# Optimization experiments

Hardware: AMD Instinct MI355X
Metric: run time of the kernel (lower is better)

## Reference

```python
import jax, jax.numpy as jnp
import numpy as np


def setup_inputs() -> dict:
    key = jax.random.key(0)
    ks = jax.random.split(key, 8)
    B, C, H, W = 4, 256, 64, 64
    C8 = C // 8
    s = 0.05
    return {
        "x": jax.random.normal(ks[0], (B, C, H, W), jnp.float32),
        "wq": jax.random.normal(ks[1], (C8, C), jnp.float32) * s,
        "bq": jax.random.normal(ks[2], (C8,), jnp.float32) * s,
        "wk": jax.random.normal(ks[3], (C8, C), jnp.float32) * s,
        "bk": jax.random.normal(ks[4], (C8,), jnp.float32) * s,
        "wv": jax.random.normal(ks[5], (C, C), jnp.float32) * s,
        "bv": jax.random.normal(ks[6], (C,), jnp.float32) * s,
        "gamma": jax.random.uniform(ks[7], (1,), jnp.float32),
    }


def reference(x, wq, bq, wk, bk, wv, bv, gamma):
    B, C, H, W = x.shape
    N = H * W
    xf = x.reshape(B, C, N)  # flatten spatial: [B, C, N]
    # 1x1 convs are channel-wise matmuls
    q = jnp.einsum("dc,bcn->bnd", wq, xf) + bq[None, None, :]  # [B, N, C/8]
    k = jnp.einsum("dc,bcn->bdn", wk, xf) + bk[None, :, None]  # [B, C/8, N]
    v = jnp.einsum("dc,bcn->bdn", wv, xf) + bv[None, :, None]  # [B, C, N]
    energy = jnp.einsum("bnd,bdm->bnm", q, k)  # [B, N, N]
    attention = jax.nn.softmax(energy, axis=-1)
    # out = value @ attention^T  -> [B, C, N]
    out = jnp.einsum("bcm,bnm->bcn", v, attention)
    out = out.reshape(B, C, H, W)
    return gamma[0] * out + x
```

## Files before the change

kernel.cpp:

```cpp
#include <hip/hip_runtime.h>
#include <hip/hip_bf16.h>
#include <stdint.h>

#define B_ 4
#define C_ 256
#define N_ 4096
#define D_ 32
#define KT 512

typedef __bf16 bf16_t;
typedef __bf16 bf16x4_t __attribute__((ext_vector_type(4)));
typedef __bf16 bf16x8_t __attribute__((ext_vector_type(8)));
typedef float  f32x4    __attribute__((ext_vector_type(4)));

__global__ __launch_bounds__(256) void cast_w_kernel(
    const float* __restrict__ wq, const float* __restrict__ wk,
    const float* __restrict__ wv, bf16_t* __restrict__ Wb)
{
  const int gr = blockIdx.x;
  const int t  = threadIdx.x;
  float v;
  if (gr < 32)      v = wq[gr * C_ + t];
  else if (gr < 64) v = wk[(gr - 32) * C_ + t];
  else              v = wv[(gr - 64) * C_ + t];
  Wb[gr * C_ + t] = (bf16_t)v;
}

__global__ __launch_bounds__(256) void proj_kernel(
    const float* __restrict__ x, const bf16_t* __restrict__ Wb,
    const float* __restrict__ bq, const float* __restrict__ bk,
    const float* __restrict__ bv,
    bf16_t* __restrict__ Qh, bf16_t* __restrict__ Kh, bf16_t* __restrict__ Vh)
{
  __shared__ float xs[64][65];
  const int bi = blockIdx.x;
  const int b  = bi & 3;
  const int n0 = (bi >> 2) * 64;
  const int t = threadIdx.x, w = t >> 6, lane = t & 63;
  const int l4 = lane >> 4, lm = lane & 15;

  const f32x4 z4 = {0.f, 0.f, 0.f, 0.f};
  f32x4 acc[5][4];
#pragma unroll
  for (int rt = 0; rt < 5; ++rt)
#pragma unroll
    for (int ct = 0; ct < 4; ++ct) acc[rt][ct] = z4;

  const int lr = t >> 2;
  const int lc = (t & 3) * 16;

#pragma unroll 1
  for (int k0 = 0; k0 < C_; k0 += 64) {
    __syncthreads();
#pragma unroll
    for (int i = 0; i < 4; ++i) {
      const f32x4 v = *(const f32x4*)(x + ((size_t)(b * C_ + k0 + lr)) * N_ + n0 + lc + i * 4);
      xs[lr][lc + i * 4 + 0] = v[0];
      xs[lr][lc + i * 4 + 1] = v[1];
      xs[lr][lc + i * 4 + 2] = v[2];
      xs[lr][lc + i * 4 + 3] = v[3];
    }
    __syncthreads();

    bf16x8_t af[5][2], bfr[4][2];
#pragma unroll
    for (int rt = 0; rt < 5; ++rt)
#pragma unroll
      for (int kc = 0; kc < 2; ++kc)
        af[rt][kc] = *(const bf16x8_t*)(Wb + (size_t)(w * 80 + rt * 16 + lm) * C_ + k0 + kc * 32 + l4 * 8);
#pragma unroll
    for (int ct = 0; ct < 4; ++ct)
#pragma unroll
      for (int kc = 0; kc < 2; ++kc) {
        bf16_t tmp[8];
#pragma unroll
        for (int j = 0; j < 8; ++j)
          tmp[j] = (bf16_t)xs[kc * 32 + l4 * 8 + j][ct * 16 + lm];
        bfr[ct][kc] = *(bf16x8_t*)tmp;
      }
#pragma unroll
    for (int rt = 0; rt < 5; ++rt)
#pragma unroll
      for (int ct = 0; ct < 4; ++ct)
#pragma unroll
        for (int kc = 0; kc < 2; ++kc)
          acc[rt][ct] = __builtin_amdgcn_mfma_f32_16x16x32_bf16(af[rt][kc], bfr[ct][kc], acc[rt][ct], 0, 0, 0);
  }

#pragma unroll
  for (int rt = 0; rt < 5; ++rt)
#pragma unroll
    for (int r = 0; r < 4; ++r) {
      const int gr = w * 80 + rt * 16 + 4 * l4 + r;
      const float bias = (gr < 32) ? bq[gr] : (gr < 64) ? bk[gr - 32] : bv[gr - 64];
#pragma unroll
      for (int ct = 0; ct < 4; ++ct) {
        const int n = n0 + ct * 16 + lm;
        float v = acc[rt][ct][r] + bias;
        if (gr < 32) {
          v *= 1.44269504088896f;
          Qh[((size_t)(b * N_ + n)) * D_ + gr] = (bf16_t)v;
        } else if (gr < 64) {
          Kh[((size_t)(b * N_ + n)) * D_ + (gr - 32)] = (bf16_t)v;
        } else {
          Vh[((size_t)(b * C_ + (gr - 64))) * N_ + n] = (bf16_t)v;
        }
      }
    }
}

__global__ __launch_bounds__(512, 2) void attn_kernel(
    const bf16_t* __restrict__ Qh, const bf16_t* __restrict__ Kh,
    const bf16_t* __restrict__ Vh, const float* __restrict__ x,
    const float* __restrict__ gamma, float* __restrict__ out)
{
  __shared__ __align__(16) bf16_t Pl[2][64][KT];
  __shared__ __align__(16) float  Lx[64][12];

  const int bi = blockIdx.x;
  const int xcd = bi & 7, slot = bi >> 3;
  const int b  = xcd >> 1;
  const int q0 = ((xcd & 1) * 32 + slot) * 64;

  const int t = threadIdx.x, w = t >> 6, lane = t & 63;
  const int l4 = lane >> 4, lm = lane & 15;
  const int swz = (lm & 7) << 3;

  const f32x4 z4 = {0.f, 0.f, 0.f, 0.f};

  bf16x8_t qf[4];
#pragma unroll
  for (int rt = 0; rt < 4; ++rt)
    qf[rt] = *(const bf16x8_t*)(Qh + ((size_t)(b * N_ + q0 + rt * 16 + lm)) * D_ + l4 * 8);

  const bf16_t* kbase = Kh + ((size_t)(b * N_ + w * 64 + lm)) * D_ + l4 * 8;
  const bf16_t* vbase = Vh + ((size_t)(b * C_ + w * 32 + lm)) * N_ + l4 * 8;

  f32x4 acc[2][4];
#pragma unroll
  for (int ct = 0; ct < 2; ++ct)
#pragma unroll
    for (int rt = 0; rt < 4; ++rt) acc[ct][rt] = z4;
  float l_run[4] = {0.f, 0.f, 0.f, 0.f};

  bf16x8_t kf[4], kn[4];
#pragma unroll
  for (int mt = 0; mt < 4; ++mt)
    kf[mt] = *(const bf16x8_t*)(kbase + (size_t)(mt * 16) * D_);
  bf16x8_t vf0[2][2], vf1[2][2];
#pragma unroll
  for (int ct = 0; ct < 2; ++ct)
#pragma unroll
    for (int kc = 0; kc < 2; ++kc) {
      vf0[ct][kc] = *(const bf16x8_t*)(vbase + (size_t)(ct * 16) * N_ + kc * 32);
      vf1[ct][kc] = *(const bf16x8_t*)(vbase + (size_t)(ct * 16) * N_ + 64 + kc * 32);
    }

#pragma unroll 1
  for (int it = 0; it < N_ / KT; ++it) {
    const int buf = it & 1;

    f32x4 S[4][4];
#pragma unroll
    for (int rt = 0; rt < 4; ++rt)
#pragma unroll
      for (int mt = 0; mt < 4; ++mt)
        S[rt][mt] = __builtin_amdgcn_mfma_f32_16x16x32_bf16(kf[mt], qf[rt], z4, 0, 0, 0);

    const int k0n = ((it + 1) * KT) & (N_ - 1);
#pragma unroll
    for (int mt = 0; mt < 4; ++mt)
      kn[mt] = *(const bf16x8_t*)(kbase + (size_t)(k0n + mt * 16) * D_);

#pragma unroll
    for (int rt = 0; rt < 4; ++rt) {
      const int prow = rt * 16 + lm;
#pragma unroll
      for (int mt = 0; mt < 4; ++mt) {
        const float p0 = __builtin_amdgcn_exp2f(S[rt][mt][0]);
        const float p1 = __builtin_amdgcn_exp2f(S[rt][mt][1]);
        const float p2 = __builtin_amdgcn_exp2f(S[rt][mt][2]);
        const float p3 = __builtin_amdgcn_exp2f(S[rt][mt][3]);
        l_run[rt] += (p0 + p1) + (p2 + p3);
        bf16x4_t w4 = {(bf16_t)p0, (bf16_t)p1, (bf16_t)p2, (bf16_t)p3};
        *(bf16x4_t*)&Pl[buf][prow][(w * 64 + mt * 16 + 4 * l4) ^ swz] = w4;
      }
    }

    asm volatile("s_waitcnt lgkmcnt(0)" ::: "memory");
    __builtin_amdgcn_s_barrier();

#pragma unroll
    for (int s4 = 0; s4 < 8; ++s4) {
      bf16x8_t pa[4][2];
#pragma unroll
      for (int rt = 0; rt < 4; ++rt)
#pragma unroll
        for (int kc = 0; kc < 2; ++kc)
          pa[rt][kc] = *(const bf16x8_t*)&Pl[buf][rt * 16 + lm][(s4 * 64 + kc * 32 + l4 * 8) ^ swz];
      const int knx = (it * KT + (s4 + 2) * 64) & (N_ - 1);
      if ((s4 & 1) == 0) {
#pragma unroll
        for (int ct = 0; ct < 2; ++ct)
#pragma unroll
          for (int kc = 0; kc < 2; ++kc)
#pragma unroll
            for (int rt = 0; rt < 4; ++rt)
              acc[ct][rt] = __builtin_amdgcn_mfma_f32_16x16x32_bf16(vf0[ct][kc], pa[rt][kc], acc[ct][rt], 0, 0, 0);
#pragma unroll
        for (int ct = 0; ct < 2; ++ct)
#pragma unroll
          for (int kc = 0; kc < 2; ++kc)
            vf0[ct][kc] = *(const bf16x8_t*)(vbase + (size_t)(ct * 16) * N_ + knx + kc * 32);
      } else {
#pragma unroll
        for (int ct = 0; ct < 2; ++ct)
#pragma unroll
          for (int kc = 0; kc < 2; ++kc)
#pragma unroll
            for (int rt = 0; rt < 4; ++rt)
              acc[ct][rt] = __builtin_amdgcn_mfma_f32_16x16x32_bf16(vf1[ct][kc], pa[rt][kc], acc[ct][rt], 0, 0, 0);
#pragma unroll
        for (int ct = 0; ct < 2; ++ct)
#pragma unroll
          for (int kc = 0; kc < 2; ++kc)
            vf1[ct][kc] = *(const bf16x8_t*)(vbase + (size_t)(ct * 16) * N_ + knx + kc * 32);
      }
    }

#pragma unroll
    for (int mt = 0; mt < 4; ++mt) kf[mt] = kn[mt];
  }

#pragma unroll
  for (int rt = 0; rt < 4; ++rt) {
    l_run[rt] += __shfl_xor(l_run[rt], 16);
    l_run[rt] += __shfl_xor(l_run[rt], 32);
  }
  if (l4 == 0) {
#pragma unroll
    for (int rt = 0; rt < 4; ++rt) Lx[rt * 16 + lm][w] = l_run[rt];
  }
  asm volatile("s_waitcnt lgkmcnt(0)" ::: "memory");
  __builtin_amdgcn_s_barrier();

  const float g = gamma[0];
#pragma unroll
  for (int rt = 0; rt < 4; ++rt) {
    const f32x4 s0 = *(const f32x4*)&Lx[rt * 16 + lm][0];
    const f32x4 s1 = *(const f32x4*)&Lx[rt * 16 + lm][4];
    const float lt = ((s0[0] + s0[1]) + (s0[2] + s0[3])) + ((s1[0] + s1[1]) + (s1[2] + s1[3]));
    const float inv = 1.f / lt;
    const int n = q0 + rt * 16 + lm;
#pragma unroll
    for (int ct = 0; ct < 2; ++ct) {
#pragma unroll
      for (int r = 0; r < 4; ++r) {
        const int c = w * 32 + ct * 16 + 4 * l4 + r;
        const size_t idx = ((size_t)(b * C_ + c)) * N_ + n;
        out[idx] = g * (acc[ct][rt][r] * inv) + x[idx];
      }
    }
  }
}

extern "C" void kernel_launch(void* const* d_in, const int* in_sizes, int n_in,
                              void* d_out, int out_size, void* d_ws, size_t ws_size,
                              hipStream_t stream) {
  const float* x     = (const float*)d_in[0];
  const float* wq    = (const float*)d_in[1];
  const float* bq    = (const float*)d_in[2];
  const float* wk    = (const float*)d_in[3];
  const float* bk    = (const float*)d_in[4];
  const float* wv    = (const float*)d_in[5];
  const float* bv    = (const float*)d_in[6];
  const float* gamma = (const float*)d_in[7];
  float* out = (float*)d_out;

  bf16_t* Qh = (bf16_t*)d_ws;
  bf16_t* Kh = Qh + (size_t)B_ * N_ * D_;
  bf16_t* Vh = Kh + (size_t)B_ * N_ * D_;
  bf16_t* Wb = Vh + (size_t)B_ * C_ * N_;

  cast_w_kernel<<<320, 256, 0, stream>>>(wq, wk, wv, Wb);
  proj_kernel<<<256, 256, 0, stream>>>(x, Wb, bq, bk, bv, Qh, Kh, Vh);
  attn_kernel<<<256, 512, 0, stream>>>(Qh, Kh, Vh, x, gamma, out);
}
```

Baseline: 93.12 us.

## Split attention work across 16 waves with key-split PV and LDS reduction

Doubles the attention block to 1024 threads and halves the key tile to 256. Each wave now computes one 16-key slice of the score tile instead of 64 keys. In the PV stage, wave pairs split the key dimension, and their partial accumulators are reduced through LDS before the epilogue. The aim is more waves in flight per CU to hide latency, at the cost of twice as many barriers per key, fewer MFMAs between barriers, an extra reduction pass, and the loss of the 2-blocks-per-CU occupancy hint.

```diff
diff --git a/kernel.cpp b/kernel.cpp
--- a/kernel.cpp
+++ b/kernel.cpp
@@ -6,7 +6,7 @@
 #define C_ 256
 #define N_ 4096
 #define D_ 32
-#define KT 512
+#define KT 256
 
 typedef __bf16 bf16_t;
 typedef __bf16 bf16x4_t __attribute__((ext_vector_type(4)));
@@ -109,13 +109,13 @@
     }
 }
 
-__global__ __launch_bounds__(512, 2) void attn_kernel(
+__global__ __launch_bounds__(1024) void attn_kernel(
     const bf16_t* __restrict__ Qh, const bf16_t* __restrict__ Kh,
     const bf16_t* __restrict__ Vh, const float* __restrict__ x,
     const float* __restrict__ gamma, float* __restrict__ out)
 {
   __shared__ __align__(16) bf16_t Pl[2][64][KT];
-  __shared__ __align__(16) float  Lx[64][12];
+  __shared__ __align__(16) float  Lx[64][20];
 
   const int bi = blockIdx.x;
   const int xcd = bi & 7, slot = bi >> 3;
@@ -124,6 +124,7 @@
 
   const int t = threadIdx.x, w = t >> 6, lane = t & 63;
   const int l4 = lane >> 4, lm = lane & 15;
+  const int cg = w >> 1, kh = w & 1;
   const int swz = (lm & 7) << 3;
 
   const f32x4 z4 = {0.f, 0.f, 0.f, 0.f};
@@ -133,8 +134,8 @@
   for (int rt = 0; rt < 4; ++rt)
     qf[rt] = *(const bf16x8_t*)(Qh + ((size_t)(b * N_ + q0 + rt * 16 + lm)) * D_ + l4 * 8);
 
-  const bf16_t* kbase = Kh + ((size_t)(b * N_ + w * 64 + lm)) * D_ + l4 * 8;
-  const bf16_t* vbase = Vh + ((size_t)(b * C_ + w * 32 + lm)) * N_ + l4 * 8;
+  const bf16_t* kbase = Kh + ((size_t)(b * N_ + w * 16 + lm)) * D_ + l4 * 8;
+  const bf16_t* vbase = Vh + ((size_t)(b * C_ + cg * 32 + lm)) * N_ + kh * 128 + l4 * 8;
 
   f32x4 acc[2][4];
 #pragma unroll
@@ -143,93 +144,72 @@
     for (int rt = 0; rt < 4; ++rt) acc[ct][rt] = z4;
   float l_run[4] = {0.f, 0.f, 0.f, 0.f};
 
-  bf16x8_t kf[4], kn[4];
-#pragma unroll
-  for (int mt = 0; mt < 4; ++mt)
-    kf[mt] = *(const bf16x8_t*)(kbase + (size_t)(mt * 16) * D_);
-  bf16x8_t vf0[2][2], vf1[2][2];
-#pragma unroll
-  for (int ct = 0; ct < 2; ++ct)
-#pragma unroll
-    for (int kc = 0; kc < 2; ++kc) {
-      vf0[ct][kc] = *(const bf16x8_t*)(vbase + (size_t)(ct * 16) * N_ + kc * 32);
-      vf1[ct][kc] = *(const bf16x8_t*)(vbase + (size_t)(ct * 16) * N_ + 64 + kc * 32);
-    }
+  bf16x8_t kf;
+  kf = *(const bf16x8_t*)(kbase);
+  bf16x8_t vf0[2], vf1[2];
+#pragma unroll
+  for (int ct = 0; ct < 2; ++ct) {
+    vf0[ct] = *(const bf16x8_t*)(vbase + (size_t)(ct * 16) * N_);
+    vf1[ct] = *(const bf16x8_t*)(vbase + (size_t)(ct * 16) * N_ + 32);
+  }
 
 #pragma unroll 1
   for (int it = 0; it < N_ / KT; ++it) {
     const int buf = it & 1;
 
-    f32x4 S[4][4];
+    f32x4 S[4];
 #pragma unroll
     for (int rt = 0; rt < 4; ++rt)
-#pragma unroll
-      for (int mt = 0; mt < 4; ++mt)
-        S[rt][mt] = __builtin_amdgcn_mfma_f32_16x16x32_bf16(kf[mt], qf[rt], z4, 0, 0, 0);
+      S[rt] = __builtin_amdgcn_mfma_f32_16x16x32_bf16(kf, qf[rt], z4, 0, 0, 0);
 
     const int k0n = ((it + 1) * KT) & (N_ - 1);
-#pragma unroll
-    for (int mt = 0; mt < 4; ++mt)
-      kn[mt] = *(const bf16x8_t*)(kbase + (size_t)(k0n + mt * 16) * D_);
+    bf16x8_t kn = *(const bf16x8_t*)(kbase + (size_t)k0n * D_);
 
 #pragma unroll
     for (int rt = 0; rt < 4; ++rt) {
       const int prow = rt * 16 + lm;
-#pragma unroll
-      for (int mt = 0; mt < 4; ++mt) {
-        const float p0 = __builtin_amdgcn_exp2f(S[rt][mt][0]);
-        const float p1 = __builtin_amdgcn_exp2f(S[rt][mt][1]);
-        const float p2 = __builtin_amdgcn_exp2f(S[rt][mt][2]);
-        const float p3 = __builtin_amdgcn_exp2f(S[rt][mt][3]);
-        l_run[rt] += (p0 + p1) + (p2 + p3);
-        bf16x4_t w4 = {(bf16_t)p0, (bf16_t)p1, (bf16_t)p2, (bf16_t)p3};
-        *(bf16x4_t*)&Pl[buf][prow][(w * 64 + mt * 16 + 4 * l4) ^ swz] = w4;
-      }
+      const float p0 = __builtin_amdgcn_exp2f(S[rt][0]);
+      const float p1 = __builtin_amdgcn_exp2f(S[rt][1]);
+      const float p2 = __builtin_amdgcn_exp2f(S[rt][2]);
+      const float p3 = __builtin_amdgcn_exp2f(S[rt][3]);
+      l_run[rt] += (p0 + p1) + (p2 + p3);
+      bf16x4_t w4 = {(bf16_t)p0, (bf16_t)p1, (bf16_t)p2, (bf16_t)p3};
+      *(bf16x4_t*)&Pl[buf][prow][(w * 16 + 4 * l4) ^ swz] = w4;
     }
 
     asm volatile("s_waitcnt lgkmcnt(0)" ::: "memory");
     __builtin_amdgcn_s_barrier();
 
 #pragma unroll
-    for (int s4 = 0; s4 < 8; ++s4) {
-      bf16x8_t pa[4][2];
+    for (int s4 = 0; s4 < 4; ++s4) {
+      bf16x8_t pa[4];
 #pragma unroll
       for (int rt = 0; rt < 4; ++rt)
-#pragma unroll
-        for (int kc = 0; kc < 2; ++kc)
-          pa[rt][kc] = *(const bf16x8_t*)&Pl[buf][rt * 16 + lm][(s4 * 64 + kc * 32 + l4 * 8) ^ swz];
-      const int knx = (it * KT + (s4 + 2) * 64) & (N_ - 1);
+        pa[rt] = *(const bf16x8_t*)&Pl[buf][rt * 16 + lm][(kh * 128 + s4 * 32 + l4 * 8) ^ swz];
+      const int knx = (it * KT + (s4 + 2) * 32) & 127;
+      const int kbase_nx = ((it + (s4 >= 2)) * KT) & (N_ - 1);
       if ((s4 & 1) == 0) {
 #pragma unroll
         for (int ct = 0; ct < 2; ++ct)
 #pragma unroll
-          for (int kc = 0; kc < 2; ++kc)
-#pragma unroll
-            for (int rt = 0; rt < 4; ++rt)
-              acc[ct][rt] = __builtin_amdgcn_mfma_f32_16x16x32_bf16(vf0[ct][kc], pa[rt][kc], acc[ct][rt], 0, 0, 0);
-#pragma unroll
-        for (int ct = 0; ct < 2; ++ct)
-#pragma unroll
-          for (int kc = 0; kc < 2; ++kc)
-            vf0[ct][kc] = *(const bf16x8_t*)(vbase + (size_t)(ct * 16) * N_ + knx + kc * 32);
+          for (int rt = 0; rt < 4; ++rt)
+            acc[ct][rt] = __builtin_amdgcn_mfma_f32_16x16x32_bf16(vf0[ct], pa[rt], acc[ct][rt], 0, 0, 0);
+#pragma unroll
+        for (int ct = 0; ct < 2; ++ct)
+          vf0[ct] = *(const bf16x8_t*)(vbase + (size_t)(ct * 16) * N_ + kbase_nx + knx);
       } else {
 #pragma unroll
         for (int ct = 0; ct < 2; ++ct)
 #pragma unroll
-          for (int kc = 0; kc < 2; ++kc)
-#pragma unroll
-            for (int rt = 0; rt < 4; ++rt)
-              acc[ct][rt] = __builtin_amdgcn_mfma_f32_16x16x32_bf16(vf1[ct][kc], pa[rt][kc], acc[ct][rt], 0, 0, 0);
-#pragma unroll
-        for (int ct = 0; ct < 2; ++ct)
-#pragma unroll
-          for (int kc = 0; kc < 2; ++kc)
-            vf1[ct][kc] = *(const bf16x8_t*)(vbase + (size_t)(ct * 16) * N_ + knx + kc * 32);
-      }
-    }
-
-#pragma unroll
-    for (int mt = 0; mt < 4; ++mt) kf[mt] = kn[mt];
+          for (int rt = 0; rt < 4; ++rt)
+            acc[ct][rt] = __builtin_amdgcn_mfma_f32_16x16x32_bf16(vf1[ct], pa[rt], acc[ct][rt], 0, 0, 0);
+#pragma unroll
+        for (int ct = 0; ct < 2; ++ct)
+          vf1[ct] = *(const bf16x8_t*)(vbase + (size_t)(ct * 16) * N_ + kbase_nx + knx);
+      }
+    }
+
+    kf = kn;
   }
 
 #pragma unroll
@@ -241,24 +221,42 @@
 #pragma unroll
     for (int rt = 0; rt < 4; ++rt) Lx[rt * 16 + lm][w] = l_run[rt];
   }
+
+  float* Ax = (float*)&Pl[0][0][0];
   asm volatile("s_waitcnt lgkmcnt(0)" ::: "memory");
   __builtin_amdgcn_s_barrier();
 
-  const float g = gamma[0];
-#pragma unroll
-  for (int rt = 0; rt < 4; ++rt) {
-    const f32x4 s0 = *(const f32x4*)&Lx[rt * 16 + lm][0];
-    const f32x4 s1 = *(const f32x4*)&Lx[rt * 16 + lm][4];
-    const float lt = ((s0[0] + s0[1]) + (s0[2] + s0[3])) + ((s1[0] + s1[1]) + (s1[2] + s1[3]));
-    const float inv = 1.f / lt;
-    const int n = q0 + rt * 16 + lm;
-#pragma unroll
-    for (int ct = 0; ct < 2; ++ct) {
-#pragma unroll
-      for (int r = 0; r < 4; ++r) {
-        const int c = w * 32 + ct * 16 + 4 * l4 + r;
-        const size_t idx = ((size_t)(b * C_ + c)) * N_ + n;
-        out[idx] = g * (acc[ct][rt][r] * inv) + x[idx];
+  if (kh == 1) {
+#pragma unroll
+    for (int rt = 0; rt < 4; ++rt)
+#pragma unroll
+      for (int ct = 0; ct < 2; ++ct)
+        *(f32x4*)&Ax[((cg * 64) + rt * 16 + lm) * 32 + ct * 16 + 4 * l4] = acc[ct][rt];
+  }
+  asm volatile("s_waitcnt lgkmcnt(0)" ::: "memory");
+  __builtin_amdgcn_s_barrier();
+
+  if (kh == 0) {
+    const float g = gamma[0];
+#pragma unroll
+    for (int rt = 0; rt < 4; ++rt) {
+      const f32x4 s0 = *(const f32x4*)&Lx[rt * 16 + lm][0];
+      const f32x4 s1 = *(const f32x4*)&Lx[rt * 16 + lm][4];
+      const f32x4 s2 = *(const f32x4*)&Lx[rt * 16 + lm][8];
+      const f32x4 s3 = *(const f32x4*)&Lx[rt * 16 + lm][12];
+      const float lt = (((s0[0] + s0[1]) + (s0[2] + s0[3])) + ((s1[0] + s1[1]) + (s1[2] + s1[3]))) +
+                       (((s2[0] + s2[1]) + (s2[2] + s2[3])) + ((s3[0] + s3[1]) + (s3[2] + s3[3])));
+      const float inv = 1.f / lt;
+      const int n = q0 + rt * 16 + lm;
+#pragma unroll
+      for (int ct = 0; ct < 2; ++ct) {
+        const f32x4 other = *(const f32x4*)&Ax[((cg * 64) + rt * 16 + lm) * 32 + ct * 16 + 4 * l4];
+#pragma unroll
+        for (int r = 0; r < 4; ++r) {
+          const int c = cg * 32 + ct * 16 + 4 * l4 + r;
+          const size_t idx = ((size_t)(b * C_ + c)) * N_ + n;
+          out[idx] = g * ((acc[ct][rt][r] + other[r]) * inv) + x[idx];
+        }
       }
     }
   }
@@ -284,5 +282,5 @@
 
   cast_w_kernel<<<320, 256, 0, stream>>>(wq, wk, wv, Wb);
   proj_kernel<<<256, 256, 0, stream>>>(x, Wb, bq, bk, bv, Qh, Kh, Vh);
-  attn_kernel<<<256, 512, 0, stream>>>(Qh, Kh, Vh, x, gamma, out);
-}
+  attn_kernel<<<256, 1024, 0, stream>>>(Qh, Kh, Vh, x, gamma, out);
+}
```

Result: slower. 96.36 us (+3.5%).

## Software-pipeline QK^T and exp with PV MFMAs using halved key tile

Applied to the files above, without the earlier changes.

Halves the key tile to 256 and restructures the main loop so that the next tile's QK^T MFMAs and exp/P-store run interleaved with the current tile's PV MFMAs. A prologue computes the first P tile and an epilogue drains the last. The intent is to overlap transcendental and LDS-write work with matrix-core work and to need only one barrier per smaller tile. In exchange the loop has more iterations and more barriers overall, and the staged S registers raise register pressure.

```diff
diff --git a/kernel.cpp b/kernel.cpp
--- a/kernel.cpp
+++ b/kernel.cpp
@@ -6,7 +6,7 @@
 #define C_ 256
 #define N_ 4096
 #define D_ 32
-#define KT 512
+#define KT 256
 
 typedef __bf16 bf16_t;
 typedef __bf16 bf16x4_t __attribute__((ext_vector_type(4)));
@@ -133,7 +133,7 @@
   for (int rt = 0; rt < 4; ++rt)
     qf[rt] = *(const bf16x8_t*)(Qh + ((size_t)(b * N_ + q0 + rt * 16 + lm)) * D_ + l4 * 8);
 
-  const bf16_t* kbase = Kh + ((size_t)(b * N_ + w * 64 + lm)) * D_ + l4 * 8;
+  const bf16_t* kbase = Kh + ((size_t)(b * N_ + w * 32 + lm)) * D_ + l4 * 8;
   const bf16_t* vbase = Vh + ((size_t)(b * C_ + w * 32 + lm)) * N_ + l4 * 8;
 
   f32x4 acc[2][4];
@@ -143,10 +143,13 @@
     for (int rt = 0; rt < 4; ++rt) acc[ct][rt] = z4;
   float l_run[4] = {0.f, 0.f, 0.f, 0.f};
 
-  bf16x8_t kf[4], kn[4];
-#pragma unroll
-  for (int mt = 0; mt < 4; ++mt)
+  bf16x8_t kf[2], kn[2];
+#pragma unroll
+  for (int mt = 0; mt < 2; ++mt)
     kf[mt] = *(const bf16x8_t*)(kbase + (size_t)(mt * 16) * D_);
+#pragma unroll
+  for (int mt = 0; mt < 2; ++mt)
+    kn[mt] = *(const bf16x8_t*)(kbase + (size_t)(KT + mt * 16) * D_);
   bf16x8_t vf0[2][2], vf1[2][2];
 #pragma unroll
   for (int ct = 0; ct < 2; ++ct)
@@ -156,49 +159,171 @@
       vf1[ct][kc] = *(const bf16x8_t*)(vbase + (size_t)(ct * 16) * N_ + 64 + kc * 32);
     }
 
+  f32x4 S[4][2];
+#pragma unroll
+  for (int rt = 0; rt < 4; ++rt)
+#pragma unroll
+    for (int mt = 0; mt < 2; ++mt)
+      S[rt][mt] = __builtin_amdgcn_mfma_f32_16x16x32_bf16(kf[mt], qf[rt], z4, 0, 0, 0);
+#pragma unroll
+  for (int rt = 0; rt < 4; ++rt) {
+    const int prow = rt * 16 + lm;
+#pragma unroll
+    for (int mt = 0; mt < 2; ++mt) {
+      const float p0 = __builtin_amdgcn_exp2f(S[rt][mt][0]);
+      const float p1 = __builtin_amdgcn_exp2f(S[rt][mt][1]);
+      const float p2 = __builtin_amdgcn_exp2f(S[rt][mt][2]);
+      const float p3 = __builtin_amdgcn_exp2f(S[rt][mt][3]);
+      l_run[rt] += (p0 + p1) + (p2 + p3);
+      bf16x4_t w4 = {(bf16_t)p0, (bf16_t)p1, (bf16_t)p2, (bf16_t)p3};
+      *(bf16x4_t*)&Pl[0][prow][(w * 32 + mt * 16 + 4 * l4) ^ swz] = w4;
+    }
+  }
+  asm volatile("s_waitcnt lgkmcnt(0)" ::: "memory");
+  __builtin_amdgcn_s_barrier();
+
 #pragma unroll 1
-  for (int it = 0; it < N_ / KT; ++it) {
+  for (int it = 0; it < N_ / KT - 1; ++it) {
     const int buf = it & 1;
-
-    f32x4 S[4][4];
+    bf16x8_t pa[4][2];
+
 #pragma unroll
     for (int rt = 0; rt < 4; ++rt)
 #pragma unroll
-      for (int mt = 0; mt < 4; ++mt)
-        S[rt][mt] = __builtin_amdgcn_mfma_f32_16x16x32_bf16(kf[mt], qf[rt], z4, 0, 0, 0);
-
-    const int k0n = ((it + 1) * KT) & (N_ - 1);
-#pragma unroll
-    for (int mt = 0; mt < 4; ++mt)
-      kn[mt] = *(const bf16x8_t*)(kbase + (size_t)(k0n + mt * 16) * D_);
-
-#pragma unroll
-    for (int rt = 0; rt < 4; ++rt) {
+      for (int kc = 0; kc < 2; ++kc)
+        pa[rt][kc] = *(const bf16x8_t*)&Pl[buf][rt * 16 + lm][(0 * 64 + kc * 32 + l4 * 8) ^ swz];
+#pragma unroll
+    for (int rt = 0; rt < 4; ++rt)
+#pragma unroll
+      for (int mt = 0; mt < 2; ++mt)
+        S[rt][mt] = __builtin_amdgcn_mfma_f32_16x16x32_bf16(kn[mt], qf[rt], z4, 0, 0, 0);
+#pragma unroll
+    for (int ct = 0; ct < 2; ++ct)
+#pragma unroll
+      for (int kc = 0; kc < 2; ++kc)
+#pragma unroll
+        for (int rt = 0; rt < 4; ++rt)
+          acc[ct][rt] = __builtin_amdgcn_mfma_f32_16x16x32_bf16(vf0[ct][kc], pa[rt][kc], acc[ct][rt], 0, 0, 0);
+    {
+      const int knx = (it * KT + 2 * 64) & (N_ - 1);
+#pragma unroll
+      for (int ct = 0; ct < 2; ++ct)
+#pragma unroll
+        for (int kc = 0; kc < 2; ++kc)
+          vf0[ct][kc] = *(const bf16x8_t*)(vbase + (size_t)(ct * 16) * N_ + knx + kc * 32);
+    }
+
+#pragma unroll
+    for (int rt = 0; rt < 4; ++rt)
+#pragma unroll
+      for (int kc = 0; kc < 2; ++kc)
+        pa[rt][kc] = *(const bf16x8_t*)&Pl[buf][rt * 16 + lm][(1 * 64 + kc * 32 + l4 * 8) ^ swz];
+#pragma unroll
+    for (int rt = 0; rt < 2; ++rt) {
       const int prow = rt * 16 + lm;
 #pragma unroll
-      for (int mt = 0; mt < 4; ++mt) {
+      for (int mt = 0; mt < 2; ++mt) {
         const float p0 = __builtin_amdgcn_exp2f(S[rt][mt][0]);
         const float p1 = __builtin_amdgcn_exp2f(S[rt][mt][1]);
         const float p2 = __builtin_amdgcn_exp2f(S[rt][mt][2]);
         const float p3 = __builtin_amdgcn_exp2f(S[rt][mt][3]);
         l_run[rt] += (p0 + p1) + (p2 + p3);
         bf16x4_t w4 = {(bf16_t)p0, (bf16_t)p1, (bf16_t)p2, (bf16_t)p3};
-        *(bf16x4_t*)&Pl[buf][prow][(w * 64 + mt * 16 + 4 * l4) ^ swz] = w4;
-      }
+        *(bf16x4_t*)&Pl[buf ^ 1][prow][(w * 32 + mt * 16 + 4 * l4) ^ swz] = w4;
+      }
+    }
+#pragma unroll
+    for (int ct = 0; ct < 2; ++ct)
+#pragma unroll
+      for (int kc = 0; kc < 2; ++kc)
+#pragma unroll
+        for (int rt = 0; rt < 4; ++rt)
+          acc[ct][rt] = __builtin_amdgcn_mfma_f32_16x16x32_bf16(vf1[ct][kc], pa[rt][kc], acc[ct][rt], 0, 0, 0);
+    {
+      const int knx = (it * KT + 3 * 64) & (N_ - 1);
+#pragma unroll
+      for (int ct = 0; ct < 2; ++ct)
+#pragma unroll
+        for (int kc = 0; kc < 2; ++kc)
+          vf1[ct][kc] = *(const bf16x8_t*)(vbase + (size_t)(ct * 16) * N_ + knx + kc * 32);
+    }
+
+#pragma unroll
+    for (int rt = 0; rt < 4; ++rt)
+#pragma unroll
+      for (int kc = 0; kc < 2; ++kc)
+        pa[rt][kc] = *(const bf16x8_t*)&Pl[buf][rt * 16 + lm][(2 * 64 + kc * 32 + l4 * 8) ^ swz];
+#pragma unroll
+    for (int rt = 2; rt < 4; ++rt) {
+      const int prow = rt * 16 + lm;
+#pragma unroll
+      for (int mt = 0; mt < 2; ++mt) {
+        const float p0 = __builtin_amdgcn_exp2f(S[rt][mt][0]);
+        const float p1 = __builtin_amdgcn_exp2f(S[rt][mt][1]);
+        const float p2 = __builtin_amdgcn_exp2f(S[rt][mt][2]);
+        const float p3 = __builtin_amdgcn_exp2f(S[rt][mt][3]);
+        l_run[rt] += (p0 + p1) + (p2 + p3);
+        bf16x4_t w4 = {(bf16_t)p0, (bf16_t)p1, (bf16_t)p2, (bf16_t)p3};
+        *(bf16x4_t*)&Pl[buf ^ 1][prow][(w * 32 + mt * 16 + 4 * l4) ^ swz] = w4;
+      }
+    }
+#pragma unroll
+    for (int ct = 0; ct < 2; ++ct)
+#pragma unroll
+      for (int kc = 0; kc < 2; ++kc)
+#pragma unroll
+        for (int rt = 0; rt < 4; ++rt)
+          acc[ct][rt] = __builtin_amdgcn_mfma_f32_16x16x32_bf16(vf0[ct][kc], pa[rt][kc], acc[ct][rt], 0, 0, 0);
+    {
+      const int knx = (it * KT + 4 * 64) & (N_ - 1);
+#pragma unroll
+      for (int ct = 0; ct < 2; ++ct)
+#pragma unroll
+        for (int kc = 0; kc < 2; ++kc)
+          vf0[ct][kc] = *(const bf16x8_t*)(vbase + (size_t)(ct * 16) * N_ + knx + kc * 32);
+    }
+
+#pragma unroll
+    for (int rt = 0; rt < 4; ++rt)
+#pragma unroll
+      for (int kc = 0; kc < 2; ++kc)
+        pa[rt][kc] = *(const bf16x8_t*)&Pl[buf][rt * 16 + lm][(3 * 64 + kc * 32 + l4 * 8) ^ swz];
+    {
+      const int k0n = ((it + 2) * KT) & (N_ - 1);
+#pragma unroll
+      for (int mt = 0; mt < 2; ++mt)
+        kn[mt] = *(const bf16x8_t*)(kbase + (size_t)(k0n + mt * 16) * D_);
+    }
+#pragma unroll
+    for (int ct = 0; ct < 2; ++ct)
+#pragma unroll
+      for (int kc = 0; kc < 2; ++kc)
+#pragma unroll
+        for (int rt = 0; rt < 4; ++rt)
+          acc[ct][rt] = __builtin_amdgcn_mfma_f32_16x16x32_bf16(vf1[ct][kc], pa[rt][kc], acc[ct][rt], 0, 0, 0);
+    {
+      const int knx = (it * KT + 5 * 64) & (N_ - 1);
+#pragma unroll
+      for (int ct = 0; ct < 2; ++ct)
+#pragma unroll
+        for (int kc = 0; kc < 2; ++kc)
+          vf1[ct][kc] = *(const bf16x8_t*)(vbase + (size_t)(ct * 16) * N_ + knx + kc * 32);
     }
 
     asm volatile("s_waitcnt lgkmcnt(0)" ::: "memory");
     __builtin_amdgcn_s_barrier();
-
-#pragma unroll
-    for (int s4 = 0; s4 < 8; ++s4) {
+  }
+
+  {
+    const int buf = (N_ / KT - 1) & 1;
+#pragma unroll
+    for (int s4 = 0; s4 < 4; ++s4) {
       bf16x8_t pa[4][2];
 #pragma unroll
       for (int rt = 0; rt < 4; ++rt)
 #pragma unroll
         for (int kc = 0; kc < 2; ++kc)
           pa[rt][kc] = *(const bf16x8_t*)&Pl[buf][rt * 16 + lm][(s4 * 64 + kc * 32 + l4 * 8) ^ swz];
-      const int knx = (it * KT + (s4 + 2) * 64) & (N_ - 1);
       if ((s4 & 1) == 0) {
 #pragma unroll
         for (int ct = 0; ct < 2; ++ct)
@@ -207,11 +332,6 @@
 #pragma unroll
             for (int rt = 0; rt < 4; ++rt)
               acc[ct][rt] = __builtin_amdgcn_mfma_f32_16x16x32_bf16(vf0[ct][kc], pa[rt][kc], acc[ct][rt], 0, 0, 0);
-#pragma unroll
-        for (int ct = 0; ct < 2; ++ct)
-#pragma unroll
-          for (int kc = 0; kc < 2; ++kc)
-            vf0[ct][kc] = *(const bf16x8_t*)(vbase + (size_t)(ct * 16) * N_ + knx + kc * 32);
       } else {
 #pragma unroll
         for (int ct = 0; ct < 2; ++ct)
@@ -220,16 +340,24 @@
 #pragma unroll
             for (int rt = 0; rt < 4; ++rt)
               acc[ct][rt] = __builtin_amdgcn_mfma_f32_16x16x32_bf16(vf1[ct][kc], pa[rt][kc], acc[ct][rt], 0, 0, 0);
-#pragma unroll
-        for (int ct = 0; ct < 2; ++ct)
-#pragma unroll
-          for (int kc = 0; kc < 2; ++kc)
-            vf1[ct][kc] = *(const bf16x8_t*)(vbase + (size_t)(ct * 16) * N_ + knx + kc * 32);
-      }
-    }
-
-#pragma unroll
-    for (int mt = 0; mt < 4; ++mt) kf[mt] = kn[mt];
+      }
+      if (s4 < 2) {
+        const int knx = ((N_ / KT - 1) * KT + (s4 + 2) * 64) & (N_ - 1);
+        if ((s4 & 1) == 0) {
+#pragma unroll
+          for (int ct = 0; ct < 2; ++ct)
+#pragma unroll
+            for (int kc = 0; kc < 2; ++kc)
+              vf0[ct][kc] = *(const bf16x8_t*)(vbase + (size_t)(ct * 16) * N_ + knx + kc * 32);
+        } else {
+#pragma unroll
+          for (int ct = 0; ct < 2; ++ct)
+#pragma unroll
+            for (int kc = 0; kc < 2; ++kc)
+              vf1[ct][kc] = *(const bf16x8_t*)(vbase + (size_t)(ct * 16) * N_ + knx + kc * 32);
+        }
+      }
+    }
   }
 
 #pragma unroll
```

Result: no change. 92.95 us (-0.2%).
